# Optimization experiments

Hardware: AMD Instinct MI355X
Metric: run time of the kernel (lower is better)

## Reference

```python
import jax, jax.numpy as jnp
import numpy as np

B, T, D, H, NC, PS = 128, 256, 6, 512, 4, 12


def setup_inputs() -> dict:
    key = jax.random.key(0)
    ks = jax.random.split(key, 24)
    s = 1.0 / np.sqrt(H)
    u = lambda k, shape: jax.random.uniform(k, shape, jnp.float32, -s, s)
    inp = {
        'x': jax.random.normal(ks[0], (B, T, D), jnp.float32),
        # encoder LSTM (layer0 input D, layer1 input H); torch gate order i,f,g,o
        'enc_Wih0': u(ks[1], (4 * H, D)), 'enc_Whh0': u(ks[2], (4 * H, H)),
        'enc_bih0': u(ks[3], (4 * H,)),   'enc_bhh0': u(ks[4], (4 * H,)),
        'enc_Wih1': u(ks[5], (4 * H, H)), 'enc_Whh1': u(ks[6], (4 * H, H)),
        'enc_bih1': u(ks[7], (4 * H,)),   'enc_bhh1': u(ks[8], (4 * H,)),
        # decoder LSTM (both layers input H)
        'dec_Wih0': u(ks[9], (4 * H, H)),  'dec_Whh0': u(ks[10], (4 * H, H)),
        'dec_bih0': u(ks[11], (4 * H,)),   'dec_bhh0': u(ks[12], (4 * H,)),
        'dec_Wih1': u(ks[13], (4 * H, H)), 'dec_Whh1': u(ks[14], (4 * H, H)),
        'dec_bih1': u(ks[15], (4 * H,)),   'dec_bhh1': u(ks[16], (4 * H,)),
        # heads
        'fc_W': u(ks[17], (D, H)),  'fc_b': u(ks[18], (D,)),
        'cls_W': u(ks[19], (NC, H)), 'cls_b': u(ks[20], (NC,)),
        'reg_W': u(ks[21], (1, H)),  'reg_b': u(ks[22], (1,)),
    }
    return inp


def _cell(inp, h, c, Wih, Whh, bih, bhh):
    g = inp @ Wih.T + h @ Whh.T + bih + bhh  # [B,4H]
    i, f, gg, o = jnp.split(g, 4, axis=-1)
    c = jax.nn.sigmoid(f) * c + jax.nn.sigmoid(i) * jnp.tanh(gg)
    h = jax.nn.sigmoid(o) * jnp.tanh(c)
    return h, c


def _lstm_layer(x, Wih, Whh, bih, bhh):
    # x: [B,T,in] -> precompute input projections once: [T,B,4H]
    xg = jnp.einsum('bti,gi->tbg', x, Wih) + bih + bhh
    h0 = jnp.zeros((x.shape[0], H), x.dtype)
    c0 = jnp.zeros((x.shape[0], H), x.dtype)
    def step(carry, g_t):
        h, c = carry
        g = g_t + h @ Whh.T
        i, f, gg, o = jnp.split(g, 4, axis=-1)
        c = jax.nn.sigmoid(f) * c + jax.nn.sigmoid(i) * jnp.tanh(gg)
        h = jax.nn.sigmoid(o) * jnp.tanh(c)
        return (h, c), h
    (hT, cT), ys = jax.lax.scan(step, (h0, c0), xg)
    return jnp.transpose(ys, (1, 0, 2)), hT, cT  # [B,T,H]


def reference(x, enc_Wih0, enc_Whh0, enc_bih0, enc_bhh0,
              enc_Wih1, enc_Whh1, enc_bih1, enc_bhh1,
              dec_Wih0, dec_Whh0, dec_bih0, dec_bhh0,
              dec_Wih1, dec_Whh1, dec_bih1, dec_bhh1,
              fc_W, fc_b, cls_W, cls_b, reg_W, reg_b):
    out0, h0f, c0f = _lstm_layer(x, enc_Wih0, enc_Whh0, enc_bih0, enc_bhh0)
    out1, h1f, c1f = _lstm_layer(out0, enc_Wih1, enc_Whh1, enc_bih1, enc_bhh1)
    last = out1[:, -1, :]                      # [B,H]
    class_logits = last @ cls_W.T + cls_b      # [B,NC]
    time_regression = (last @ reg_W.T + reg_b)[:, 0]  # [B]
    def dstep(carry, _):
        h0, c0, h1, c1, inp = carry
        h0n, c0n = _cell(inp, h0, c0, dec_Wih0, dec_Whh0, dec_bih0, dec_bhh0)
        h1n, c1n = _cell(h0n, h1, c1, dec_Wih1, dec_Whh1, dec_bih1, dec_bhh1)
        pred = h1n @ fc_W.T + fc_b  # [B,D]
        return (h0n, c0n, h1n, c1n, h1n), pred
    init = (h0f, c0f, h1f, c1f, last)
    _, preds = jax.lax.scan(dstep, init, None, length=PS)  # [PS,B,D]
    forecast = jnp.transpose(preds, (1, 0, 2))             # [B,PS,D]
    return forecast, class_logits, time_regression
```

## Files before the change

### kernel.cpp

```cpp
#include <hip/hip_runtime.h>
#include <hip/hip_bf16.h>

typedef __attribute__((ext_vector_type(8))) short short8;
typedef __attribute__((ext_vector_type(4))) float floatx4;
typedef unsigned short u16;
typedef unsigned long long u64;

#define SCOPE_AGENT __HIP_MEMORY_SCOPE_AGENT


__device__ __forceinline__ u16 f2b(float f){
  union { float fl; unsigned u; } v; v.fl = f;
  unsigned r = v.u + 0x7fffu + ((v.u >> 16) & 1u);
  return (u16)(r >> 16);
}
__device__ __forceinline__ float b2f(u16 b){
  union { unsigned u; float f; } v; v.u = ((unsigned)b) << 16; return v.f;
}

__device__ __forceinline__ short8 ldc8(const u16* p){
  short8 r;
  asm volatile("global_load_dwordx4 %0, %1, off sc1" : "=&v"(r) : "v"(p));
  return r;
}
__device__ __forceinline__ void stc64(u64* p, u64 v){
  __hip_atomic_store(p, v, __ATOMIC_RELAXED, SCOPE_AGENT);
}

__device__ __forceinline__ bool expired(long long t0){
  return (wall_clock64() - t0) > 50000000LL;
}


__global__ void reorder_w_k(const float* __restrict__ W, u16* __restrict__ out){
  int idx = blockIdx.x*256 + threadIdx.x;
  int r = idx >> 9, k = idx & 511;
  int rp = ((r & 511) << 2) | (r >> 9);
  out[rp*512 + k] = f2b(W[idx]);
}
__global__ void prep_wx0_k(const float* __restrict__ W, u16* __restrict__ out){
  int idx = blockIdx.x*256 + threadIdx.x;
  int r = idx >> 5, k = idx & 31;
  int rp = ((r & 511) << 2) | (r >> 9);
  out[rp*32 + k] = (k < 6) ? f2b(W[r*6 + k]) : (u16)0;
}
__global__ void prep_bias_k(const float* __restrict__ bih, const float* __restrict__ bhh,
                            float* __restrict__ out){
  int r = blockIdx.x*256 + threadIdx.x;
  int rp = ((r & 511) << 2) | (r >> 9);
  out[rp] = bih[r] + bhh[r];
}
__global__ void prep_x_k(const float* __restrict__ x, u16* __restrict__ out){
  int idx = blockIdx.x*256 + threadIdx.x;
  int t = idx >> 12; int rem = idx & 4095; int b = rem >> 5; int k = rem & 31;
  out[idx] = (k < 6) ? f2b(x[(b*256 + t)*6 + k]) : (u16)0;
}
__global__ void init_out_k(float* __restrict__ out, const float* __restrict__ fcb,
                           const float* __restrict__ clsb, const float* __restrict__ regb){
  int i = blockIdx.x*256 + threadIdx.x;
  if (i < 9216)       out[i] = fcb[i % 6];
  else if (i < 9728)  out[i] = clsb[(i - 9216) & 3];
  else if (i < 9856)  out[i] = regb[0];
}


struct PK {
  const u16 *Xb, *Wx0, *W0hh, *W1ih, *W1hh, *Wd0ih, *Wd0hh, *Wd1ih, *Wd1hh;
  const float *Bs;
  u16 *h0b, *h1b;
  unsigned *F;
  const float *fcW, *clsW, *regW;
  float *out;
};

#define HB 65536

__device__ __forceinline__ void pollF(const unsigned* F, int bg, int thr0, int thr1,
                                      long long t0){
  const int lane = threadIdx.x & 63;
  const unsigned* ap = (lane < 32) ? (F + bg*32 + lane)
                                   : (F + 128 + bg*32 + (lane - 32));
  const int thr = (lane < 32) ? thr0 : thr1;
  for(;;){
    int v = (int)__hip_atomic_load(ap, __ATOMIC_RELAXED, SCOPE_AGENT);
    if (__all(v >= thr)) return;
    if (expired(t0)) return;
    if (__any((thr - v) > 2)) __builtin_amdgcn_s_sleep(16);
    else                      __builtin_amdgcn_s_sleep(1);
  }
}

template<int NK1, bool COH1>
__device__ __forceinline__ void lstm_step(
    const u16* __restrict__ A1, int a1rowlen, const u16* __restrict__ ldsW1, int st1,
    const u16* __restrict__ A2, const u16* __restrict__ ldsW2,
    const float* __restrict__ biasp, u16* __restrict__ hdst,
    float* creg, float (*g)[69], float* hout,
    int bg, int nt, int wv, int lane)
{
  const int lrow = lane & 15, kq = lane >> 4;
  const int arow = bg*32 + wv*16 + lrow;
  short8 a1[NK1], a2[16];
  {
    const u16* p1 = A1 + arow*a1rowlen + kq*8;
    #pragma unroll
    for (int k = 0; k < NK1; ++k)
      a1[k] = COH1 ? ldc8(p1 + k*32) : *(const short8*)(p1 + k*32);
    const u16* p2 = A2 + arow*512 + kq*8;
    #pragma unroll
    for (int k = 0; k < 16; ++k) a2[k] = ldc8(p2 + k*32);
  }
  asm volatile("s_waitcnt vmcnt(0)" ::: "memory");
  __builtin_amdgcn_sched_barrier(0);
  floatx4 acc[4];
  #pragma unroll
  for (int nn = 0; nn < 4; ++nn) acc[nn] = (floatx4){0.f,0.f,0.f,0.f};
  #pragma unroll
  for (int nn = 0; nn < 4; ++nn){
    const u16* wb = ldsW1 + (nn*16 + lrow)*st1 + kq*8;
    #pragma unroll
    for (int k = 0; k < NK1; ++k)
      acc[nn] = __builtin_amdgcn_mfma_f32_16x16x32_bf16(a1[k], *(const short8*)(wb + k*32), acc[nn], 0,0,0);
  }
  #pragma unroll
  for (int nn = 0; nn < 4; ++nn){
    const u16* wb = ldsW2 + (nn*16 + lrow)*520 + kq*8;
    #pragma unroll
    for (int k = 0; k < 16; ++k)
      acc[nn] = __builtin_amdgcn_mfma_f32_16x16x32_bf16(a2[k], *(const short8*)(wb + k*32), acc[nn], 0,0,0);
  }
  #pragma unroll
  for (int nn = 0; nn < 4; ++nn){
    float bn = biasp[nn*16 + lrow];
    #pragma unroll
    for (int r = 0; r < 4; ++r)
      g[wv*16 + kq*4 + r][nn*16 + lrow] = acc[nn][r] + bn;
  }
  __builtin_amdgcn_wave_barrier();
  const int bl = lane >> 2, jq = lane & 3;
  const float* gr = g[wv*16 + bl];
  union { u16 h[4]; u64 q; } pk;
  #pragma unroll
  for (int jj = 0; jj < 4; ++jj){
    int cb = (jq*4 + jj)*4;
    float gi = gr[cb+0], gf = gr[cb+1], gg = gr[cb+2], go = gr[cb+3];
    float iv = 1.f/(1.f + expf(-gi));
    float fv = 1.f/(1.f + expf(-gf));
    float ov = 1.f/(1.f + expf(-go));
    float cn = fv*creg[jj] + iv*tanhf(gg);
    creg[jj] = cn;
    pk.h[jj] = f2b(ov * tanhf(cn));
    hout[jj] = b2f(pk.h[jj]);
  }
  stc64((u64*)(hdst + (bg*32 + wv*16 + bl)*512 + nt*16 + jq*4), pk.q);
}


__global__ __launch_bounds__(128, 1) __attribute__((amdgpu_waves_per_eu(1, 1)))
void persist_k(PK p){
  const int w = blockIdx.x, tid = threadIdx.x;
  const int wv = tid >> 6, lane = tid & 63;
  const long long t0 = wall_clock64();
  __shared__ float g[32][69];
  extern __shared__ u16 dynW[];
  unsigned* F = p.F;

  const int role = w >> 7;
  const int bg   = (w >> 5) & 3;
  const int nt   = w & 31;
  const int fidx = role*128 + bg*32 + nt;
  u16* WA = dynW;
  u16* WB = dynW + 64*520;
  float creg[4] = {0.f,0.f,0.f,0.f};
  float hout[4];

  auto setflag = [&](unsigned val){
    __syncthreads();
    if (tid == 0) __hip_atomic_store(F + fidx, val, __ATOMIC_RELAXED, SCOPE_AGENT);
  };

  if (role == 0){
    {
      const unsigned* sA = (const unsigned*)(p.Wx0 + nt*64*32);
      unsigned* dA = (unsigned*)WA;
      for (int i = tid; i < 64*16; i += 128){ int r = i>>4, c = i&15; dA[r*20+c] = sA[r*16+c]; }
      const unsigned* sB = (const unsigned*)(p.W0hh + (size_t)nt*64*512);
      unsigned* dB = (unsigned*)WB;
      for (int i = tid; i < 64*256; i += 128){ int r = i>>8, c = i&255; dB[r*260+c] = sB[r*256+c]; }
    }
    const float* biasp = p.Bs + nt*64;
    __syncthreads();
    for (int t = 0; t < 256; ++t){
      if (wv == 0) pollF(F, bg, t, t-3, t0);
      __syncthreads();
      lstm_step<1,false>(p.Xb + t*4096, 32, WA, 40,
                         p.h0b + ((t+3)&3)*HB, WB,
                         biasp, p.h0b + (t&3)*HB, creg, g, hout, bg, nt, wv, lane);
      setflag(t+1);
    }
    {
      const unsigned* sA = (const unsigned*)(p.Wd0ih + (size_t)nt*64*512);
      const unsigned* sB = (const unsigned*)(p.Wd0hh + (size_t)nt*64*512);
      unsigned* dA = (unsigned*)WA; unsigned* dB = (unsigned*)WB;
      for (int i = tid; i < 64*256; i += 128){
        int r = i>>8, c = i&255;
        dA[r*260+c] = sA[r*256+c]; dB[r*260+c] = sB[r*256+c];
      }
    }
    biasp = p.Bs + 4096 + nt*64;
    __syncthreads();
    for (int s = 0; s < 12; ++s){
      if (wv == 0) pollF(F, bg, 256+s, 256+s, t0);
      __syncthreads();
      lstm_step<16,true>(p.h1b + ((s+3)&3)*HB, 512, WA, 520,
                         p.h0b + ((s+3)&3)*HB, WB,
                         biasp, p.h0b + (s&3)*HB, creg, g, hout, bg, nt, wv, lane);
      setflag(257+s);
    }
  } else {
    {
      const unsigned* sA = (const unsigned*)(p.W1ih + (size_t)nt*64*512);
      const unsigned* sB = (const unsigned*)(p.W1hh + (size_t)nt*64*512);
      unsigned* dA = (unsigned*)WA; unsigned* dB = (unsigned*)WB;
      for (int i = tid; i < 64*256; i += 128){
        int r = i>>8, c = i&255;
        dA[r*260+c] = sA[r*256+c]; dB[r*260+c] = sB[r*256+c];
      }
    }
    const float* biasp = p.Bs + 2048 + nt*64;
    __syncthreads();
    const int batch = bg*32 + wv*16 + (lane >> 2);
    const int jq = lane & 3;
    for (int u = 0; u < 256; ++u){
      if (wv == 0) pollF(F, bg, u+1, u, t0);
      __syncthreads();
      lstm_step<16,true>(p.h0b + (u&3)*HB, 512, WA, 520,
                         p.h1b + ((u+3)&3)*HB, WB,
                         biasp, p.h1b + (u&3)*HB, creg, g, hout, bg, nt, wv, lane);
      if (u == 255){
        float a[5] = {0.f,0.f,0.f,0.f,0.f};
        #pragma unroll
        for (int jj = 0; jj < 4; ++jj){
          int col = nt*16 + jq*4 + jj;
          float hv = hout[jj];
          a[0] += hv * p.clsW[col];
          a[1] += hv * p.clsW[512 + col];
          a[2] += hv * p.clsW[1024 + col];
          a[3] += hv * p.clsW[1536 + col];
          a[4] += hv * p.regW[col];
        }
        #pragma unroll
        for (int c = 0; c < 4; ++c) atomicAdd(&p.out[9216 + batch*4 + c], a[c]);
        atomicAdd(&p.out[9728 + batch], a[4]);
      }
      setflag(u+1);
    }
    {
      const unsigned* sA = (const unsigned*)(p.Wd1ih + (size_t)nt*64*512);
      const unsigned* sB = (const unsigned*)(p.Wd1hh + (size_t)nt*64*512);
      unsigned* dA = (unsigned*)WA; unsigned* dB = (unsigned*)WB;
      for (int i = tid; i < 64*256; i += 128){
        int r = i>>8, c = i&255;
        dA[r*260+c] = sA[r*256+c]; dB[r*260+c] = sB[r*256+c];
      }
    }
    biasp = p.Bs + 6144 + nt*64;
    __syncthreads();
    for (int s = 0; s < 12; ++s){
      if (wv == 0) pollF(F, bg, 257+s, 256+s, t0);
      __syncthreads();
      lstm_step<16,true>(p.h0b + (s&3)*HB, 512, WA, 520,
                         p.h1b + ((s+3)&3)*HB, WB,
                         biasp, p.h1b + (s&3)*HB, creg, g, hout, bg, nt, wv, lane);
      #pragma unroll
      for (int d = 0; d < 6; ++d){
        float ad = 0.f;
        #pragma unroll
        for (int jj = 0; jj < 4; ++jj)
          ad += hout[jj] * p.fcW[d*512 + nt*16 + jq*4 + jj];
        atomicAdd(&p.out[batch*72 + s*6 + d], ad);
      }
      setflag(257+s);
    }
  }
}


extern "C" void kernel_launch(void* const* d_in, const int* in_sizes, int n_in,
                              void* d_out, int out_size, void* d_ws, size_t ws_size,
                              hipStream_t stream){
  const float* x     = (const float*)d_in[0];
  const float* eWih0 = (const float*)d_in[1];
  const float* eWhh0 = (const float*)d_in[2];
  const float* ebih0 = (const float*)d_in[3];
  const float* ebhh0 = (const float*)d_in[4];
  const float* eWih1 = (const float*)d_in[5];
  const float* eWhh1 = (const float*)d_in[6];
  const float* ebih1 = (const float*)d_in[7];
  const float* ebhh1 = (const float*)d_in[8];
  const float* dWih0 = (const float*)d_in[9];
  const float* dWhh0 = (const float*)d_in[10];
  const float* dbih0 = (const float*)d_in[11];
  const float* dbhh0 = (const float*)d_in[12];
  const float* dWih1 = (const float*)d_in[13];
  const float* dWhh1 = (const float*)d_in[14];
  const float* dbih1 = (const float*)d_in[15];
  const float* dbhh1 = (const float*)d_in[16];
  const float* fcW   = (const float*)d_in[17];
  const float* fcb   = (const float*)d_in[18];
  const float* clsW  = (const float*)d_in[19];
  const float* clsb  = (const float*)d_in[20];
  const float* regW  = (const float*)d_in[21];
  const float* regb  = (const float*)d_in[22];
  float* out = (float*)d_out;

  uintptr_t base = (uintptr_t)d_ws;
  auto carve = [&](size_t n)->void*{
    void* p = (void*)base; base += (n + 255) & ~(size_t)255; return p;
  };
  u16* Wx0b  = (u16*)carve(2048*32*2);
  u16* We0hh = (u16*)carve(2048*512*2);
  u16* We1ih = (u16*)carve(2048*512*2);
  u16* We1hh = (u16*)carve(2048*512*2);
  u16* Wd0ih = (u16*)carve(2048*512*2);
  u16* Wd0hh = (u16*)carve(2048*512*2);
  u16* Wd1ih = (u16*)carve(2048*512*2);
  u16* Wd1hh = (u16*)carve(2048*512*2);
  float* Bs  = (float*)carve(4*2048*4);
  u16* Xb    = (u16*)carve(256*128*32*2);
  u16* h0b   = (u16*)carve((size_t)4*HB*2);
  u16* h1b   = (u16*)carve((size_t)4*HB*2);
  unsigned* F = (unsigned*)carve(256*4);

  (void)hipMemsetAsync(h0b, 0, (size_t)4*HB*2 + (size_t)4*HB*2 + 1024, stream);

  reorder_w_k<<<4096,256,0,stream>>>(eWhh0, We0hh);
  reorder_w_k<<<4096,256,0,stream>>>(eWih1, We1ih);
  reorder_w_k<<<4096,256,0,stream>>>(eWhh1, We1hh);
  reorder_w_k<<<4096,256,0,stream>>>(dWih0, Wd0ih);
  reorder_w_k<<<4096,256,0,stream>>>(dWhh0, Wd0hh);
  reorder_w_k<<<4096,256,0,stream>>>(dWih1, Wd1ih);
  reorder_w_k<<<4096,256,0,stream>>>(dWhh1, Wd1hh);
  prep_wx0_k<<<256,256,0,stream>>>(eWih0, Wx0b);
  prep_bias_k<<<8,256,0,stream>>>(ebih0, ebhh0, Bs);
  prep_bias_k<<<8,256,0,stream>>>(ebih1, ebhh1, Bs + 2048);
  prep_bias_k<<<8,256,0,stream>>>(dbih0, dbhh0, Bs + 4096);
  prep_bias_k<<<8,256,0,stream>>>(dbih1, dbhh1, Bs + 6144);
  prep_x_k<<<4096,256,0,stream>>>(x, Xb);
  init_out_k<<<39,256,0,stream>>>(out, fcb, clsb, regb);

  PK p;
  p.Xb = Xb; p.Wx0 = Wx0b; p.W0hh = We0hh; p.W1ih = We1ih; p.W1hh = We1hh;
  p.Wd0ih = Wd0ih; p.Wd0hh = Wd0hh; p.Wd1ih = Wd1ih; p.Wd1hh = Wd1hh;
  p.Bs = Bs; p.h0b = h0b; p.h1b = h1b; p.F = F;
  p.fcW = fcW; p.clsW = clsW; p.regW = regW; p.out = out;

  const int dynLds = 2*64*520*2;
  (void)hipFuncSetAttribute((const void*)persist_k,
                            hipFuncAttributeMaxDynamicSharedMemorySize, dynLds);

  void* args[] = { &p };
  hipError_t e = hipLaunchCooperativeKernel((const void*)persist_k, dim3(256), dim3(128),
                                            args, dynLds, stream);
  if (e != hipSuccess){
    persist_k<<<dim3(256), dim3(128), dynLds, stream>>>(p);
  }
  (void)in_sizes; (void)n_in; (void)out_size; (void)ws_size;
}
```

Baseline: 2.487 ms.

## Split LSTM step K-reduction across two extra waves per block

```diff
diff --git a/kernel.cpp b/kernel.cpp
--- a/kernel.cpp
+++ b/kernel.cpp
@@ -95,39 +95,62 @@
     const u16* __restrict__ A1, int a1rowlen, const u16* __restrict__ ldsW1, int st1,
     const u16* __restrict__ A2, const u16* __restrict__ ldsW2,
     const float* __restrict__ biasp, u16* __restrict__ hdst,
-    float* creg, float (*g)[69], float* hout,
-    int bg, int nt, int wv, int lane)
+    float* creg, float (*g)[69], float* accX, float* hout,
+    int bg, int nt, int wv, int kh, int lane)
 {
   const int lrow = lane & 15, kq = lane >> 4;
   const int arow = bg*32 + wv*16 + lrow;
-  short8 a1[NK1], a2[16];
+  constexpr int NA1 = (NK1 == 1) ? 1 : NK1/2;
+  const int k1base = (NK1 == 1) ? 0 : kh*NA1;
+  const bool hasA1 = (NK1 > 1) || (kh == 0);
+  short8 a1[NA1], a2[8];
   {
     const u16* p1 = A1 + arow*a1rowlen + kq*8;
-    #pragma unroll
-    for (int k = 0; k < NK1; ++k)
-      a1[k] = COH1 ? ldc8(p1 + k*32) : *(const short8*)(p1 + k*32);
+    if (hasA1){
+      #pragma unroll
+      for (int k = 0; k < NA1; ++k)
+        a1[k] = COH1 ? ldc8(p1 + (k1base+k)*32) : *(const short8*)(p1 + (k1base+k)*32);
+    }
     const u16* p2 = A2 + arow*512 + kq*8;
     #pragma unroll
-    for (int k = 0; k < 16; ++k) a2[k] = ldc8(p2 + k*32);
+    for (int k = 0; k < 8; ++k) a2[k] = ldc8(p2 + (kh*8+k)*32);
   }
   asm volatile("s_waitcnt vmcnt(0)" ::: "memory");
   __builtin_amdgcn_sched_barrier(0);
   floatx4 acc[4];
   #pragma unroll
   for (int nn = 0; nn < 4; ++nn) acc[nn] = (floatx4){0.f,0.f,0.f,0.f};
-  #pragma unroll
-  for (int nn = 0; nn < 4; ++nn){
-    const u16* wb = ldsW1 + (nn*16 + lrow)*st1 + kq*8;
-    #pragma unroll
-    for (int k = 0; k < NK1; ++k)
-      acc[nn] = __builtin_amdgcn_mfma_f32_16x16x32_bf16(a1[k], *(const short8*)(wb + k*32), acc[nn], 0,0,0);
+  if (hasA1){
+    #pragma unroll
+    for (int nn = 0; nn < 4; ++nn){
+      const u16* wb = ldsW1 + (nn*16 + lrow)*st1 + kq*8;
+      #pragma unroll
+      for (int k = 0; k < NA1; ++k)
+        acc[nn] = __builtin_amdgcn_mfma_f32_16x16x32_bf16(a1[k], *(const short8*)(wb + (k1base+k)*32), acc[nn], 0,0,0);
+    }
   }
   #pragma unroll
   for (int nn = 0; nn < 4; ++nn){
     const u16* wb = ldsW2 + (nn*16 + lrow)*520 + kq*8;
     #pragma unroll
-    for (int k = 0; k < 16; ++k)
-      acc[nn] = __builtin_amdgcn_mfma_f32_16x16x32_bf16(a2[k], *(const short8*)(wb + k*32), acc[nn], 0,0,0);
+    for (int k = 0; k < 8; ++k)
+      acc[nn] = __builtin_amdgcn_mfma_f32_16x16x32_bf16(a2[k], *(const short8*)(wb + (kh*8+k)*32), acc[nn], 0,0,0);
+  }
+  if (kh == 1){
+    float* ax = accX + (wv*64 + lane)*16;
+    #pragma unroll
+    for (int nn = 0; nn < 4; ++nn)
+      #pragma unroll
+      for (int r = 0; r < 4; ++r) ax[nn*4 + r] = acc[nn][r];
+  }
+  __syncthreads();
+  if (kh == 1) return;
+  {
+    const float* ax = accX + (wv*64 + lane)*16;
+    #pragma unroll
+    for (int nn = 0; nn < 4; ++nn)
+      #pragma unroll
+      for (int r = 0; r < 4; ++r) acc[nn][r] += ax[nn*4 + r];
   }
   #pragma unroll
   for (int nn = 0; nn < 4; ++nn){
@@ -156,12 +179,14 @@
 }
 
 
-__global__ __launch_bounds__(128, 1) __attribute__((amdgpu_waves_per_eu(1, 1)))
+__global__ __launch_bounds__(256, 1) __attribute__((amdgpu_waves_per_eu(1, 1)))
 void persist_k(PK p){
   const int w = blockIdx.x, tid = threadIdx.x;
-  const int wv = tid >> 6, lane = tid & 63;
+  const int wv2 = tid >> 6, lane = tid & 63;
+  const int wv = wv2 & 1, kh = wv2 >> 1;
   const long long t0 = wall_clock64();
   __shared__ float g[32][69];
+  __shared__ float accX[2*64*16];
   extern __shared__ u16 dynW[];
   unsigned* F = p.F;
 
@@ -183,26 +208,26 @@
     {
       const unsigned* sA = (const unsigned*)(p.Wx0 + nt*64*32);
       unsigned* dA = (unsigned*)WA;
-      for (int i = tid; i < 64*16; i += 128){ int r = i>>4, c = i&15; dA[r*20+c] = sA[r*16+c]; }
+      for (int i = tid; i < 64*16; i += 256){ int r = i>>4, c = i&15; dA[r*20+c] = sA[r*16+c]; }
       const unsigned* sB = (const unsigned*)(p.W0hh + (size_t)nt*64*512);
       unsigned* dB = (unsigned*)WB;
-      for (int i = tid; i < 64*256; i += 128){ int r = i>>8, c = i&255; dB[r*260+c] = sB[r*256+c]; }
+      for (int i = tid; i < 64*256; i += 256){ int r = i>>8, c = i&255; dB[r*260+c] = sB[r*256+c]; }
     }
     const float* biasp = p.Bs + nt*64;
     __syncthreads();
     for (int t = 0; t < 256; ++t){
-      if (wv == 0) pollF(F, bg, t, t-3, t0);
+      if (wv2 == 0) pollF(F, bg, t, t-3, t0);
       __syncthreads();
       lstm_step<1,false>(p.Xb + t*4096, 32, WA, 40,
                          p.h0b + ((t+3)&3)*HB, WB,
-                         biasp, p.h0b + (t&3)*HB, creg, g, hout, bg, nt, wv, lane);
+                         biasp, p.h0b + (t&3)*HB, creg, g, accX, hout, bg, nt, wv, kh, lane);
       setflag(t+1);
     }
     {
       const unsigned* sA = (const unsigned*)(p.Wd0ih + (size_t)nt*64*512);
       const unsigned* sB = (const unsigned*)(p.Wd0hh + (size_t)nt*64*512);
       unsigned* dA = (unsigned*)WA; unsigned* dB = (unsigned*)WB;
-      for (int i = tid; i < 64*256; i += 128){
+      for (int i = tid; i < 64*256; i += 256){
         int r = i>>8, c = i&255;
         dA[r*260+c] = sA[r*256+c]; dB[r*260+c] = sB[r*256+c];
       }
@@ -210,11 +235,11 @@
     biasp = p.Bs + 4096 + nt*64;
     __syncthreads();
     for (int s = 0; s < 12; ++s){
-      if (wv == 0) pollF(F, bg, 256+s, 256+s, t0);
+      if (wv2 == 0) pollF(F, bg, 256+s, 256+s, t0);
       __syncthreads();
       lstm_step<16,true>(p.h1b + ((s+3)&3)*HB, 512, WA, 520,
                          p.h0b + ((s+3)&3)*HB, WB,
-                         biasp, p.h0b + (s&3)*HB, creg, g, hout, bg, nt, wv, lane);
+                         biasp, p.h0b + (s&3)*HB, creg, g, accX, hout, bg, nt, wv, kh, lane);
       setflag(257+s);
     }
   } else {
@@ -222,7 +247,7 @@
       const unsigned* sA = (const unsigned*)(p.W1ih + (size_t)nt*64*512);
       const unsigned* sB = (const unsigned*)(p.W1hh + (size_t)nt*64*512);
       unsigned* dA = (unsigned*)WA; unsigned* dB = (unsigned*)WB;
-      for (int i = tid; i < 64*256; i += 128){
+      for (int i = tid; i < 64*256; i += 256){
         int r = i>>8, c = i&255;
         dA[r*260+c] = sA[r*256+c]; dB[r*260+c] = sB[r*256+c];
       }
@@ -232,12 +257,12 @@
     const int batch = bg*32 + wv*16 + (lane >> 2);
     const int jq = lane & 3;
     for (int u = 0; u < 256; ++u){
-      if (wv == 0) pollF(F, bg, u+1, u, t0);
+      if (wv2 == 0) pollF(F, bg, u+1, u, t0);
       __syncthreads();
       lstm_step<16,true>(p.h0b + (u&3)*HB, 512, WA, 520,
                          p.h1b + ((u+3)&3)*HB, WB,
-                         biasp, p.h1b + (u&3)*HB, creg, g, hout, bg, nt, wv, lane);
-      if (u == 255){
+                         biasp, p.h1b + (u&3)*HB, creg, g, accX, hout, bg, nt, wv, kh, lane);
+      if (u == 255 && kh == 0){
         float a[5] = {0.f,0.f,0.f,0.f,0.f};
         #pragma unroll
         for (int jj = 0; jj < 4; ++jj){
@@ -259,7 +284,7 @@
       const unsigned* sA = (const unsigned*)(p.Wd1ih + (size_t)nt*64*512);
       const unsigned* sB = (const unsigned*)(p.Wd1hh + (size_t)nt*64*512);
       unsigned* dA = (unsigned*)WA; unsigned* dB = (unsigned*)WB;
-      for (int i = tid; i < 64*256; i += 128){
+      for (int i = tid; i < 64*256; i += 256){
         int r = i>>8, c = i&255;
         dA[r*260+c] = sA[r*256+c]; dB[r*260+c] = sB[r*256+c];
       }
@@ -267,18 +292,20 @@
     biasp = p.Bs + 6144 + nt*64;
     __syncthreads();
     for (int s = 0; s < 12; ++s){
-      if (wv == 0) pollF(F, bg, 257+s, 256+s, t0);
+      if (wv2 == 0) pollF(F, bg, 257+s, 256+s, t0);
       __syncthreads();
       lstm_step<16,true>(p.h0b + (s&3)*HB, 512, WA, 520,
                          p.h1b + ((s+3)&3)*HB, WB,
-                         biasp, p.h1b + (s&3)*HB, creg, g, hout, bg, nt, wv, lane);
-      #pragma unroll
-      for (int d = 0; d < 6; ++d){
-        float ad = 0.f;
+                         biasp, p.h1b + (s&3)*HB, creg, g, accX, hout, bg, nt, wv, kh, lane);
+      if (kh == 0){
         #pragma unroll
-        for (int jj = 0; jj < 4; ++jj)
-          ad += hout[jj] * p.fcW[d*512 + nt*16 + jq*4 + jj];
-        atomicAdd(&p.out[batch*72 + s*6 + d], ad);
+        for (int d = 0; d < 6; ++d){
+          float ad = 0.f;
+          #pragma unroll
+          for (int jj = 0; jj < 4; ++jj)
+            ad += hout[jj] * p.fcW[d*512 + nt*16 + jq*4 + jj];
+          atomicAdd(&p.out[batch*72 + s*6 + d], ad);
+        }
       }
       setflag(257+s);
     }
@@ -360,10 +387,10 @@
                             hipFuncAttributeMaxDynamicSharedMemorySize, dynLds);
 
   void* args[] = { &p };
-  hipError_t e = hipLaunchCooperativeKernel((const void*)persist_k, dim3(256), dim3(128),
+  hipError_t e = hipLaunchCooperativeKernel((const void*)persist_k, dim3(256), dim3(256),
                                             args, dynLds, stream);
   if (e != hipSuccess){
-    persist_k<<<dim3(256), dim3(128), dynLds, stream>>>(p);
+    persist_k<<<dim3(256), dim3(256), dynLds, stream>>>(p);
   }
   (void)in_sizes; (void)n_in; (void)out_size; (void)ws_size;
 }
```

New measurement: 2.186 ms. 1.14x faster.
